# Performance work log

Measured on AMD Instinct MI355X. Metric: run time of the kernel, lower is better.

## Reference

```python
import jax, jax.numpy as jnp
import numpy as np

B, N, D, D_OUT = 8, 2048, 256, 256
LN_EPS = 1e-5
LRELU_SLOPE = 0.01


def setup_inputs() -> dict:
    key = jax.random.key(0)
    ks = jax.random.split(key, 11)
    s_in = 1.0 / np.sqrt(D)
    s_out = 1.0 / np.sqrt(D)
    return {
        "x_local": jax.random.normal(ks[0], (B, N, D), dtype=jnp.float32),
        "Wq": jax.random.uniform(ks[1], (D, D), jnp.float32, -s_in, s_in),
        "bq": jax.random.uniform(ks[2], (D,), jnp.float32, -s_in, s_in),
        "Wk": jax.random.uniform(ks[3], (D, D), jnp.float32, -s_in, s_in),
        "bk": jax.random.uniform(ks[4], (D,), jnp.float32, -s_in, s_in),
        "Wv": jax.random.uniform(ks[5], (D, D), jnp.float32, -s_in, s_in),
        "bv": jax.random.uniform(ks[6], (D,), jnp.float32, -s_in, s_in),
        "Wo": jax.random.uniform(ks[7], (D_OUT, D), jnp.float32, -s_out, s_out),
        "bo": jax.random.uniform(ks[8], (D_OUT,), jnp.float32, -s_out, s_out),
        "ln_gamma": jnp.ones((D_OUT,), jnp.float32),
        "ln_beta": jnp.zeros((D_OUT,), jnp.float32),
    }


def reference(x_local, Wq, bq, Wk, bk, Wv, bv, Wo, bo, ln_gamma, ln_beta):
    # Linear layers (torch convention: y = x @ W.T + b)
    Q = jnp.einsum("bnd,ed->bne", x_local, Wq) + bq
    K = jnp.einsum("bnd,ed->bne", x_local, Wk) + bk
    V = jnp.einsum("bnd,ed->bne", x_local, Wv) + bv
    # Unscaled attention (source applies no 1/sqrt(d))
    scores = jnp.einsum("bnd,bmd->bnm", Q, K)          # [B, N, N]
    attn = jax.nn.softmax(scores, axis=-1)
    loc = jnp.einsum("bnm,bmd->bnd", attn, V)           # [B, N, D]
    # fc_out: Linear -> LayerNorm -> LeakyReLU
    h = jnp.einsum("bnd,ed->bne", loc, Wo) + bo          # [B, N, D_OUT]
    mu = jnp.mean(h, axis=-1, keepdims=True)
    var = jnp.mean(jnp.square(h - mu), axis=-1, keepdims=True)
    hn = (h - mu) / jnp.sqrt(var + LN_EPS) * ln_gamma + ln_beta
    return jnp.where(hn >= 0, hn, LRELU_SLOPE * hn)
```

## Files before the change

kernel.cpp:

```cpp
#include <hip/hip_runtime.h>

typedef unsigned short u16;
typedef __attribute__((ext_vector_type(8))) _Float16 f16x8;
typedef __attribute__((ext_vector_type(4))) float f32x4;

#define MFMA_F16 __builtin_amdgcn_mfma_f32_16x16x32_f16

static __device__ __forceinline__ u16 f2h(float f) {
    return __builtin_bit_cast(u16, (_Float16)f);
}
static __device__ __forceinline__ ushort4 f4_to_h4(const float4 v) {
    ushort4 r;
    r.x = f2h(v.x); r.y = f2h(v.y); r.z = f2h(v.z); r.w = f2h(v.w);
    return r;
}
static __device__ __forceinline__ void gl16(const u16* g, u16* l) {
    __builtin_amdgcn_global_load_lds(
        (__attribute__((address_space(1))) void*)(g),
        (__attribute__((address_space(3))) void*)(l),
        16, 0, 0);
}

__global__ __launch_bounds__(256) void prep_w(
    const float* __restrict__ wq, const float* __restrict__ wk,
    const float* __restrict__ wv, const float* __restrict__ wo,
    const float* __restrict__ x,
    u16* __restrict__ w4, u16* __restrict__ xh)
{
    const int tid = blockIdx.x * 256 + threadIdx.x;
    {
        const float* src = (tid < 16384) ? wq : (tid < 32768) ? wk
                         : (tid < 49152) ? wv : wo;
        ((ushort4*)w4)[tid] = f4_to_h4(((const float4*)src)[tid & 16383]);
    }
#pragma unroll
    for (int i = 0; i < 16; ++i) {
        const int j = i * 65536 + tid;
        ((ushort4*)xh)[j] = f4_to_h4(((const float4*)x)[j]);
    }
}

__global__ __launch_bounds__(256, 3) void proj_qkv(
    const u16* __restrict__ Xh, const u16* __restrict__ w4,
    const float* __restrict__ bq, const float* __restrict__ bk,
    const float* __restrict__ bv,
    u16* __restrict__ Qh, u16* __restrict__ Kh, u16* __restrict__ Vt)
{
    const int z = blockIdx.y;
    const u16* __restrict__ W     = w4 + z * 65536;
    const float* __restrict__ bias = (z == 0) ? bq : (z == 1) ? bk : bv;

    const int m0   = blockIdx.x * 64;
    const int t    = threadIdx.x;
    const int w    = t >> 6;
    const int lane = t & 63;
    const int quad = lane >> 4;
    const int l16  = lane & 15;

    __shared__ __align__(16) u16 smem[20480];

    const int xrow = t >> 2, xpp = t & 3;
    const unsigned xsrc = (unsigned)((m0 + xrow) * 256
                        + ((xpp ^ ((xrow >> 1) & 3)) * 8));
    unsigned wsrc[4];
#pragma unroll
    for (int i = 0; i < 4; ++i) {
        const int j = i * 256 + t;
        const int row = j >> 2, p = j & 3;
        wsrc[i] = (unsigned)(row * 256 + ((p ^ ((row >> 1) & 3)) * 8));
    }

#define PSTAGE(bufsel, kc_) do {                                             \
        u16* B_ = smem + (bufsel) * 10240;                                   \
        gl16(Xh + xsrc + (unsigned)(kc_) * 32, B_ + w * 512);                \
        _Pragma("unroll")                                                    \
        for (int i_ = 0; i_ < 4; ++i_)                                       \
            gl16(W + wsrc[i_] + (unsigned)(kc_) * 32,                        \
                 B_ + 2048 + i_ * 2048 + w * 512);                           \
    } while (0)

    f32x4 acc[16];
#pragma unroll
    for (int i = 0; i < 16; ++i) acc[i] = f32x4{0.f, 0.f, 0.f, 0.f};

    const int rp = (quad ^ ((l16 >> 1) & 3)) * 8;

    PSTAGE(0, 0);

    for (int kc = 0; kc < 8; ++kc) {
        asm volatile("s_waitcnt vmcnt(0)" ::: "memory");
        __builtin_amdgcn_s_barrier();
        __builtin_amdgcn_sched_barrier(0);
        if (kc + 1 < 8) PSTAGE((kc + 1) & 1, kc + 1);
        __builtin_amdgcn_sched_barrier(0);

        const u16* Xb = smem + (kc & 1) * 10240;
        const u16* Wb = Xb + 2048;

        const f16x8 af = *(const f16x8*)&Xb[(w * 16 + l16) * 32 + rp];
        __builtin_amdgcn_s_setprio(1);
#pragma unroll
        for (int nt = 0; nt < 16; ++nt) {
            const f16x8 bf = *(const f16x8*)&Wb[(nt * 16 + l16) * 32 + rp];
            acc[nt] = MFMA_F16(af, bf, acc[nt], 0, 0, 0);
        }
        __builtin_amdgcn_s_setprio(0);
    }
#undef PSTAGE

    __syncthreads();

    if (z < 2) {
        u16* __restrict__ Y = (z == 0) ? Qh : Kh;
#pragma unroll
        for (int nt = 0; nt < 16; ++nt) {
            const int col = nt * 16 + l16;
            const float bb = bias[col];
#pragma unroll
            for (int r = 0; r < 4; ++r)
                smem[(w * 16 + quad * 4 + r) * 264 + col] = f2h(acc[nt][r] + bb);
        }
        __syncthreads();
#pragma unroll
        for (int i = 0; i < 8; ++i) {
            const int ch = i * 256 + t;
            const int row = ch >> 5, cg = ch & 31;
            *(int4*)&Y[(size_t)(m0 + row) * 256 + cg * 8] =
                *(const int4*)&smem[row * 264 + cg * 8];
        }
    } else {
        const int b  = m0 >> 11;
        const int n0 = m0 & 2047;
#pragma unroll
        for (int nt = 0; nt < 16; ++nt) {
            const int col = nt * 16 + l16;
            const float bb = bias[col];
            ushort4 h4;
            h4.x = f2h(acc[nt][0] + bb);
            h4.y = f2h(acc[nt][1] + bb);
            h4.z = f2h(acc[nt][2] + bb);
            h4.w = f2h(acc[nt][3] + bb);
            *(ushort4*)&smem[col * 72 + w * 16 + quad * 4] = h4;
        }
        __syncthreads();
#pragma unroll
        for (int i = 0; i < 8; ++i) {
            const int ch = i * 256 + t;
            const int row = ch >> 3, cg = ch & 7;
            *(int4*)&Vt[(size_t)b * 524288 + (size_t)row * 2048 + n0 + cg * 8] =
                *(const int4*)&smem[row * 72 + cg * 8];
        }
    }
}

__global__ __launch_bounds__(512, 4) void attn(
    const u16* __restrict__ Qh, const u16* __restrict__ Kg,
    const u16* __restrict__ Vt, u16* __restrict__ Op,
    u16* __restrict__ OutS, float* __restrict__ lmpL, float* __restrict__ lmpM)
{
    const int nz = gridDim.z;
    const int z  = blockIdx.z;
    const int ntiles = 64 / nz;
    const int tile0  = ntiles * z;

    const int b  = blockIdx.y;
    const int q0 = blockIdx.x * 128;
    const int t    = threadIdx.x;
    const int w    = t >> 6;
    const int lane = t & 63;
    const int quad = lane >> 4;
    const int l16  = lane & 15;

    __shared__ __align__(16) u16 smem[34816];
    u16* Os = smem;

    f16x8 qf[8];
    {
        const size_t qrow = (size_t)(b * 2048 + q0 + w * 16 + l16) * 256;
#pragma unroll
        for (int kc = 0; kc < 8; ++kc)
            qf[kc] = *(const f16x8*)&Qh[qrow + kc * 32 + quad * 8];
    }

    unsigned kgb[2], vgb[2];
#pragma unroll
    for (int i = 0; i < 2; ++i) {
        const int j  = w * 2 + i;
        const int r  = 2 * j + (lane >> 5);
        const int pr = ((r >> 2) & 3) * 8 + (r >> 4) * 4 + (r & 3);
        const int c  = lane & 31;
        kgb[i] = (unsigned)((b * 2048 + pr) * 256 + ((c ^ (r & 7)) * 8));
        const int rp2 = 8 * j + (lane >> 3);
        const int c8 = lane & 7;
        const int d  = 2 * rp2 + (c8 >> 2);
        const int a  = (c8 & 3) ^ (rp2 & 3);
        vgb[i] = (unsigned)(b * 524288 + d * 2048 + a * 8);
    }

#define STAGE(bufsel, kt_) do {                                              \
        u16* Kb_ = smem + (bufsel) * 16384;                                  \
        u16* Vb_ = Kb_ + 8192;                                               \
        _Pragma("unroll")                                                    \
        for (int i_ = 0; i_ < 2; ++i_) {                                     \
            gl16(Kg + kgb[i_] + (unsigned)(kt_) * 256,                       \
                 Kb_ + (w * 2 + i_) * 512);                                  \
            gl16(Vt + vgb[i_] + (unsigned)(kt_),                             \
                 Vb_ + (w * 2 + i_) * 512);                                  \
        }                                                                    \
    } while (0)

    f32x4 O[16];
#pragma unroll
    for (int i = 0; i < 16; ++i) O[i] = f32x4{0.f, 0.f, 0.f, 0.f};
    float mrow = -1e30f, lrow = 0.f;

    const int vbase = (l16 >> 1) * 64 + (l16 & 1) * 32
                    + ((quad ^ ((l16 >> 1) & 3)) * 8);

    STAGE(0, tile0 * 32);

    for (int it = 0; it < ntiles; ++it) {
        asm volatile("s_waitcnt vmcnt(0)" ::: "memory");
        __builtin_amdgcn_s_barrier();
        __builtin_amdgcn_sched_barrier(0);
        if (it + 1 < ntiles) STAGE((it + 1) & 1, (tile0 + it + 1) * 32);
        __builtin_amdgcn_sched_barrier(0);

        const u16* Kc = smem + (it & 1) * 16384;
        const u16* Vc = Kc + 8192;

        f32x4 S[2];
        S[0] = f32x4{0.f, 0.f, 0.f, 0.f};
        S[1] = f32x4{0.f, 0.f, 0.f, 0.f};
        __builtin_amdgcn_s_setprio(1);
#pragma unroll
        for (int kc = 0; kc < 8; ++kc) {
#pragma unroll
            for (int kn = 0; kn < 2; ++kn) {
                const int r2 = kn * 16 + l16;
                const f16x8 kf = *(const f16x8*)
                    &Kc[r2 * 256 + (((kc * 4 + quad) ^ (l16 & 7)) * 8)];
                S[kn] = MFMA_F16(kf, qf[kc], S[kn], 0, 0, 0);
            }
        }
        __builtin_amdgcn_s_setprio(0);

        float mt = fmaxf(fmaxf(fmaxf(S[0][0], S[0][1]), fmaxf(S[0][2], S[0][3])),
                         fmaxf(fmaxf(S[1][0], S[1][1]), fmaxf(S[1][2], S[1][3])));
        mt = fmaxf(mt, __shfl_xor(mt, 16));
        mt = fmaxf(mt, __shfl_xor(mt, 32));
        if (__any(mt - mrow > 8.f)) {
            const float mnew = fmaxf(mrow, mt);
            const float a = __expf(mrow - mnew);
            lrow *= a;
#pragma unroll
            for (int dv = 0; dv < 16; ++dv)
#pragma unroll
                for (int r = 0; r < 4; ++r) O[dv][r] *= a;
            mrow = mnew;
        }
        f16x8 pfv;
        float s = 0.f;
#pragma unroll
        for (int kn = 0; kn < 2; ++kn)
#pragma unroll
            for (int r = 0; r < 4; ++r) {
                const float e = __expf(S[kn][r] - mrow);
                s += e;
                pfv[kn * 4 + r] = (_Float16)e;
            }
        s += __shfl_xor(s, 16);
        s += __shfl_xor(s, 32);
        lrow += s;

        __builtin_amdgcn_s_setprio(1);
#pragma unroll
        for (int dvt = 0; dvt < 16; ++dvt) {
            const f16x8 vf = *(const f16x8*)&Vc[dvt * 512 + vbase];
            O[dvt] = MFMA_F16(vf, pfv, O[dvt], 0, 0, 0);
        }
        __builtin_amdgcn_s_setprio(0);
    }
#undef STAGE

    __syncthreads();
    {
        const float rl = 1.0f / lrow;
#pragma unroll
        for (int dvt = 0; dvt < 16; ++dvt) {
            ushort4 h4;
            h4.x = f2h(O[dvt][0] * rl);
            h4.y = f2h(O[dvt][1] * rl);
            h4.z = f2h(O[dvt][2] * rl);
            h4.w = f2h(O[dvt][3] * rl);
            *(ushort4*)&Os[(w * 16 + l16) * 264 + dvt * 16 + quad * 4] = h4;
        }
        if (quad == 0) {
            const int grow = b * 2048 + q0 + w * 16 + l16;
            lmpL[z * 16384 + grow] = lrow;
            lmpM[z * 16384 + grow] = mrow;
        }
    }
    __syncthreads();

    {
        const int row = t >> 2;
        if (z < 2) {
            u16* __restrict__ Oz = Op + (size_t)z * 4194304;
#pragma unroll
            for (int i = 0; i < 8; ++i) {
                const int chunk = (t & 3) * 8 + i;
                *(int4*)&Oz[(size_t)(b * 2048 + q0 + row) * 256 + chunk * 8] =
                    *(const int4*)&Os[row * 264 + chunk * 8];
            }
        } else {
            u16* __restrict__ Oz = OutS + (size_t)(z - 2) * 256;
#pragma unroll
            for (int i = 0; i < 8; ++i) {
                const int chunk = (t & 3) * 8 + i;
                *(int4*)&Oz[(size_t)(b * 2048 + q0 + row) * 512 + chunk * 8] =
                    *(const int4*)&Os[row * 264 + chunk * 8];
            }
        }
    }
}

__global__ __launch_bounds__(256, 2) void outproj_ln(
    const u16* __restrict__ Op, const u16* __restrict__ OutS,
    const float* __restrict__ lmpL, const float* __restrict__ lmpM,
    const u16* __restrict__ Woh, const float* __restrict__ bo,
    const float* __restrict__ gamma, const float* __restrict__ beta,
    float* __restrict__ out)
{
    const int m0   = blockIdx.x * 32;
    const int t    = threadIdx.x;
    const int w    = t >> 6;
    const int rw   = w & 1;
    const int cw   = w >> 1;
    const int lane = t & 63;
    const int quad = lane >> 4;
    const int l16  = lane & 15;

    __shared__ __align__(16) u16 Ls[32 * 40];
    __shared__ __align__(16) u16 Ws[256 * 40];
    __shared__ _Float16 wls[4][32];
    __shared__ float part[2][16][2][2];

    if (t < 32) {
        const float l0 = lmpL[m0 + t];
        const float l1 = lmpL[16384 + m0 + t];
        const float l2 = lmpL[32768 + m0 + t];
        const float l3 = lmpL[49152 + m0 + t];
        const float m0v = lmpM[m0 + t];
        const float m1v = lmpM[16384 + m0 + t];
        const float m2v = lmpM[32768 + m0 + t];
        const float m3v = lmpM[49152 + m0 + t];
        const float mm = fmaxf(fmaxf(m0v, m1v), fmaxf(m2v, m3v));
        const float u0 = l0 * __expf(m0v - mm);
        const float u1 = l1 * __expf(m1v - mm);
        const float u2 = l2 * __expf(m2v - mm);
        const float u3 = l3 * __expf(m3v - mm);
        const float inv = 1.0f / (u0 + u1 + u2 + u3);
        wls[0][t] = (_Float16)(u0 * inv);
        wls[1][t] = (_Float16)(u1 * inv);
        wls[2][t] = (_Float16)(u2 * inv);
        wls[3][t] = (_Float16)(u3 * inv);
    }
    __syncthreads();

    f32x4 acc[8];
#pragma unroll
    for (int i = 0; i < 8; ++i) acc[i] = f32x4{0.f, 0.f, 0.f, 0.f};

    for (int kc = 0; kc < 8; ++kc) {
        if (t < 128) {
            const int row = t >> 2, cg = t & 3;
            const size_t off  = (size_t)(m0 + row) * 256 + kc * 32 + cg * 8;
            const size_t offS = (size_t)(m0 + row) * 512 + kc * 32 + cg * 8;
            const f16x8 o0 = __builtin_bit_cast(f16x8, *(const int4*)&Op[off]);
            const f16x8 o1 = __builtin_bit_cast(f16x8, *(const int4*)&Op[4194304 + off]);
            const f16x8 o2 = __builtin_bit_cast(f16x8, *(const int4*)&OutS[offS]);
            const f16x8 o3 = __builtin_bit_cast(f16x8, *(const int4*)&OutS[offS + 256]);
            const _Float16 w0 = wls[0][row], w1 = wls[1][row];
            const _Float16 w2 = wls[2][row], w3 = wls[3][row];
            f16x8 lw;
#pragma unroll
            for (int j = 0; j < 8; ++j)
                lw[j] = o0[j] * w0 + o1[j] * w1 + o2[j] * w2 + o3[j] * w3;
            *(int4*)&Ls[row * 40 + cg * 8] = __builtin_bit_cast(int4, lw);
        }
#pragma unroll
        for (int i = 0; i < 4; ++i) {
            const int ch = i * 256 + t;
            const int row = ch >> 2, cg = ch & 3;
            *(int4*)&Ws[row * 40 + cg * 8] =
                *(const int4*)&Woh[(size_t)row * 256 + kc * 32 + cg * 8];
        }
        __syncthreads();

        const f16x8 af = *(const f16x8*)&Ls[(rw * 16 + l16) * 40 + quad * 8];
#pragma unroll
        for (int nt = 0; nt < 8; ++nt) {
            const f16x8 bf = *(const f16x8*)&Ws[((cw * 8 + nt) * 16 + l16) * 40 + quad * 8];
            acc[nt] = MFMA_F16(af, bf, acc[nt], 0, 0, 0);
        }
        __syncthreads();
    }

    float g[8], bt[8], bb[8];
#pragma unroll
    for (int nt = 0; nt < 8; ++nt) {
        const int col = cw * 128 + nt * 16 + l16;
        bb[nt] = bo[col]; g[nt] = gamma[col]; bt[nt] = beta[col];
    }

    float shv[4], sh2v[4];
#pragma unroll
    for (int r = 0; r < 4; ++r) {
        float sh = 0.f, sh2 = 0.f;
#pragma unroll
        for (int nt = 0; nt < 8; ++nt) {
            const float h = acc[nt][r] + bb[nt];
            sh  += h;
            sh2 += h * h;
        }
        sh  += __shfl_xor(sh, 1);  sh  += __shfl_xor(sh, 2);
        sh  += __shfl_xor(sh, 4);  sh  += __shfl_xor(sh, 8);
        sh2 += __shfl_xor(sh2, 1); sh2 += __shfl_xor(sh2, 2);
        sh2 += __shfl_xor(sh2, 4); sh2 += __shfl_xor(sh2, 8);
        shv[r] = sh; sh2v[r] = sh2;
    }
    if (l16 == 0) {
#pragma unroll
        for (int r = 0; r < 4; ++r) {
            part[rw][quad * 4 + r][cw][0] = shv[r];
            part[rw][quad * 4 + r][cw][1] = sh2v[r];
        }
    }
    __syncthreads();

#pragma unroll
    for (int r = 0; r < 4; ++r) {
        const float sh  = shv[r]  + part[rw][quad * 4 + r][cw ^ 1][0];
        const float sh2 = sh2v[r] + part[rw][quad * 4 + r][cw ^ 1][1];
        const float mu  = sh * (1.f / 256.f);
        const float var = fmaxf(sh2 * (1.f / 256.f) - mu * mu, 0.f);
        const float rs  = rsqrtf(var + 1e-5f);
        const size_t row = (size_t)(m0 + rw * 16 + quad * 4 + r) * 256;
#pragma unroll
        for (int nt = 0; nt < 8; ++nt) {
            const float hn = (acc[nt][r] + bb[nt] - mu) * rs * g[nt] + bt[nt];
            out[row + cw * 128 + nt * 16 + l16] = (hn >= 0.f) ? hn : 0.01f * hn;
        }
    }
}

extern "C" void kernel_launch(void* const* d_in, const int* in_sizes, int n_in,
                              void* d_out, int out_size, void* d_ws, size_t ws_size,
                              hipStream_t stream)
{
    const float* x  = (const float*)d_in[0];
    const float* Wq = (const float*)d_in[1];
    const float* bq = (const float*)d_in[2];
    const float* Wk = (const float*)d_in[3];
    const float* bk = (const float*)d_in[4];
    const float* Wv = (const float*)d_in[5];
    const float* bv = (const float*)d_in[6];
    const float* Wo = (const float*)d_in[7];
    const float* bo = (const float*)d_in[8];
    const float* gm = (const float*)d_in[9];
    const float* bt = (const float*)d_in[10];
    float* out = (float*)d_out;

    u16* W4 = (u16*)d_ws;
    u16* Qh = W4 + 262144;
    u16* Kh = Qh + 4194304;
    u16* Vt = Kh + 4194304;
    u16* Op = Vt + 4194304;
    float* lmpM = (float*)(Op + 2 * 4194304);
    float* lmpL = (float*)W4;
    u16* Woh = W4 + 196608;
    u16* Xh  = (u16*)d_out;
    u16* OutS = (u16*)d_out;

    prep_w     <<<256,            256, 0, stream>>>(Wq, Wk, Wv, Wo, x, W4, Xh);
    proj_qkv   <<<dim3(256, 3),   256, 0, stream>>>(Xh, W4, bq, bk, bv, Qh, Kh, Vt);
    attn       <<<dim3(16, 8, 4), 512, 0, stream>>>(Qh, Kh, Vt, Op, OutS, lmpL, lmpM);
    outproj_ln <<<512,            256, 0, stream>>>(Op, OutS, lmpL, lmpM, Woh, bo, gm, bt, out);
}
```

Before: 185.2 us.

## Retile attention to 64-row blocks, 3-way KV split, and separate K/V staging

Attention blocks shrink to 256 threads covering 64 query rows. The KV split becomes 3-way with uneven tile counts, and a linear block-index swizzle is added. K and V loads are staged separately: K is double-buffered and V single-buffered, with extra barriers so the next V load overlaps the QK of the following tile. The output-projection merge now combines three partials instead of four. The aim is better occupancy and less LDS per block, in exchange for more barriers per tile and less V prefetch depth.

```diff
diff --git a/kernel.cpp b/kernel.cpp
--- a/kernel.cpp
+++ b/kernel.cpp
@@ -153,25 +153,29 @@
     }
 }
 
-__global__ __launch_bounds__(512, 4) void attn(
+__global__ __launch_bounds__(256, 3) void attn(
     const u16* __restrict__ Qh, const u16* __restrict__ Kg,
     const u16* __restrict__ Vt, u16* __restrict__ Op,
     u16* __restrict__ OutS, float* __restrict__ lmpL, float* __restrict__ lmpM)
 {
     const int nz = gridDim.z;
-    const int z  = blockIdx.z;
-    const int ntiles = 64 / nz;
-    const int tile0  = ntiles * z;
-
-    const int b  = blockIdx.y;
-    const int q0 = blockIdx.x * 128;
+    int lin = blockIdx.x + 32 * (blockIdx.y + 8 * blockIdx.z);
+    lin = (lin & 7) * 96 + (lin >> 3);
+    const int q0 = (lin & 31) * 64;
+    const int b  = (lin >> 5) & 7;
+    const int z  = lin >> 8;
+
+    const int tbase = 64 / nz, trem = 64 % nz;
+    const int ntiles = tbase + (z < trem ? 1 : 0);
+    const int tile0  = tbase * z + (z < trem ? z : trem);
+
     const int t    = threadIdx.x;
     const int w    = t >> 6;
     const int lane = t & 63;
     const int quad = lane >> 4;
     const int l16  = lane & 15;
 
-    __shared__ __align__(16) u16 smem[34816];
+    __shared__ __align__(16) u16 smem[24576];
     u16* Os = smem;
 
     f16x8 qf[8];
@@ -182,10 +186,10 @@
             qf[kc] = *(const f16x8*)&Qh[qrow + kc * 32 + quad * 8];
     }
 
-    unsigned kgb[2], vgb[2];
-#pragma unroll
-    for (int i = 0; i < 2; ++i) {
-        const int j  = w * 2 + i;
+    unsigned kgb[4], vgb[4];
+#pragma unroll
+    for (int i = 0; i < 4; ++i) {
+        const int j  = w * 4 + i;
         const int r  = 2 * j + (lane >> 5);
         const int pr = ((r >> 2) & 3) * 8 + (r >> 4) * 4 + (r & 3);
         const int c  = lane & 31;
@@ -197,16 +201,19 @@
         vgb[i] = (unsigned)(b * 524288 + d * 2048 + a * 8);
     }
 
-#define STAGE(bufsel, kt_) do {                                              \
-        u16* Kb_ = smem + (bufsel) * 16384;                                  \
-        u16* Vb_ = Kb_ + 8192;                                               \
+#define STAGE_K(bufsel, kt_) do {                                            \
+        u16* Kb_ = smem + (bufsel) * 8192;                                   \
         _Pragma("unroll")                                                    \
-        for (int i_ = 0; i_ < 2; ++i_) {                                     \
+        for (int i_ = 0; i_ < 4; ++i_)                                       \
             gl16(Kg + kgb[i_] + (unsigned)(kt_) * 256,                       \
-                 Kb_ + (w * 2 + i_) * 512);                                  \
+                 Kb_ + (w * 4 + i_) * 512);                                  \
+    } while (0)
+#define STAGE_V(kt_) do {                                                    \
+        u16* Vb_ = smem + 16384;                                             \
+        _Pragma("unroll")                                                    \
+        for (int i_ = 0; i_ < 4; ++i_)                                       \
             gl16(Vt + vgb[i_] + (unsigned)(kt_),                             \
-                 Vb_ + (w * 2 + i_) * 512);                                  \
-        }                                                                    \
+                 Vb_ + (w * 4 + i_) * 512);                                  \
     } while (0)
 
     f32x4 O[16];
@@ -217,17 +224,17 @@
     const int vbase = (l16 >> 1) * 64 + (l16 & 1) * 32
                     + ((quad ^ ((l16 >> 1) & 3)) * 8);
 
-    STAGE(0, tile0 * 32);
+    STAGE_K(0, tile0 * 32);
+    asm volatile("s_waitcnt vmcnt(0)" ::: "memory");
+    __builtin_amdgcn_s_barrier();
+    __builtin_amdgcn_sched_barrier(0);
+    STAGE_V(tile0 * 32);
+    if (ntiles > 1) STAGE_K(1, (tile0 + 1) * 32);
+    __builtin_amdgcn_sched_barrier(0);
 
     for (int it = 0; it < ntiles; ++it) {
-        asm volatile("s_waitcnt vmcnt(0)" ::: "memory");
-        __builtin_amdgcn_s_barrier();
-        __builtin_amdgcn_sched_barrier(0);
-        if (it + 1 < ntiles) STAGE((it + 1) & 1, (tile0 + it + 1) * 32);
-        __builtin_amdgcn_sched_barrier(0);
-
-        const u16* Kc = smem + (it & 1) * 16384;
-        const u16* Vc = Kc + 8192;
+        const u16* Kc = smem + (it & 1) * 8192;
+        const u16* Vc = smem + 16384;
 
         f32x4 S[2];
         S[0] = f32x4{0.f, 0.f, 0.f, 0.f};
@@ -273,6 +280,14 @@
         s += __shfl_xor(s, 32);
         lrow += s;
 
+        if (it + 1 < ntiles) {
+            asm volatile("s_waitcnt vmcnt(4)" ::: "memory");
+        } else {
+            asm volatile("s_waitcnt vmcnt(0)" ::: "memory");
+        }
+        __builtin_amdgcn_s_barrier();
+        __builtin_amdgcn_sched_barrier(0);
+
         __builtin_amdgcn_s_setprio(1);
 #pragma unroll
         for (int dvt = 0; dvt < 16; ++dvt) {
@@ -280,8 +295,18 @@
             O[dvt] = MFMA_F16(vf, pfv, O[dvt], 0, 0, 0);
         }
         __builtin_amdgcn_s_setprio(0);
-    }
-#undef STAGE
+
+        asm volatile("s_waitcnt vmcnt(0)" ::: "memory");
+        __builtin_amdgcn_s_barrier();
+        __builtin_amdgcn_sched_barrier(0);
+        if (it + 1 < ntiles) {
+            STAGE_V((tile0 + it + 1) * 32);
+            if (it + 2 < ntiles) STAGE_K(it & 1, (tile0 + it + 2) * 32);
+        }
+        __builtin_amdgcn_sched_barrier(0);
+    }
+#undef STAGE_K
+#undef STAGE_V
 
     __syncthreads();
     {
@@ -314,7 +339,7 @@
                     *(const int4*)&Os[row * 264 + chunk * 8];
             }
         } else {
-            u16* __restrict__ Oz = OutS + (size_t)(z - 2) * 256;
+            u16* __restrict__ Oz = OutS;
 #pragma unroll
             for (int i = 0; i < 8; ++i) {
                 const int chunk = (t & 3) * 8 + i;
@@ -343,28 +368,24 @@
 
     __shared__ __align__(16) u16 Ls[32 * 40];
     __shared__ __align__(16) u16 Ws[256 * 40];
-    __shared__ _Float16 wls[4][32];
+    __shared__ _Float16 wls[3][32];
     __shared__ float part[2][16][2][2];
 
     if (t < 32) {
         const float l0 = lmpL[m0 + t];
         const float l1 = lmpL[16384 + m0 + t];
         const float l2 = lmpL[32768 + m0 + t];
-        const float l3 = lmpL[49152 + m0 + t];
         const float m0v = lmpM[m0 + t];
         const float m1v = lmpM[16384 + m0 + t];
         const float m2v = lmpM[32768 + m0 + t];
-        const float m3v = lmpM[49152 + m0 + t];
-        const float mm = fmaxf(fmaxf(m0v, m1v), fmaxf(m2v, m3v));
+        const float mm = fmaxf(fmaxf(m0v, m1v), m2v);
         const float u0 = l0 * __expf(m0v - mm);
         const float u1 = l1 * __expf(m1v - mm);
         const float u2 = l2 * __expf(m2v - mm);
-        const float u3 = l3 * __expf(m3v - mm);
-        const float inv = 1.0f / (u0 + u1 + u2 + u3);
+        const float inv = 1.0f / (u0 + u1 + u2);
         wls[0][t] = (_Float16)(u0 * inv);
         wls[1][t] = (_Float16)(u1 * inv);
         wls[2][t] = (_Float16)(u2 * inv);
-        wls[3][t] = (_Float16)(u3 * inv);
     }
     __syncthreads();
 
@@ -380,13 +401,11 @@
             const f16x8 o0 = __builtin_bit_cast(f16x8, *(const int4*)&Op[off]);
             const f16x8 o1 = __builtin_bit_cast(f16x8, *(const int4*)&Op[4194304 + off]);
             const f16x8 o2 = __builtin_bit_cast(f16x8, *(const int4*)&OutS[offS]);
-            const f16x8 o3 = __builtin_bit_cast(f16x8, *(const int4*)&OutS[offS + 256]);
-            const _Float16 w0 = wls[0][row], w1 = wls[1][row];
-            const _Float16 w2 = wls[2][row], w3 = wls[3][row];
+            const _Float16 w0 = wls[0][row], w1 = wls[1][row], w2 = wls[2][row];
             f16x8 lw;
 #pragma unroll
             for (int j = 0; j < 8; ++j)
-                lw[j] = o0[j] * w0 + o1[j] * w1 + o2[j] * w2 + o3[j] * w3;
+                lw[j] = o0[j] * w0 + o1[j] * w1 + o2[j] * w2;
             *(int4*)&Ls[row * 40 + cg * 8] = __builtin_bit_cast(int4, lw);
         }
 #pragma unroll
@@ -485,6 +504,6 @@
 
     prep_w     <<<256,            256, 0, stream>>>(Wq, Wk, Wv, Wo, x, W4, Xh);
     proj_qkv   <<<dim3(256, 3),   256, 0, stream>>>(Xh, W4, bq, bk, bv, Qh, Kh, Vt);
-    attn       <<<dim3(16, 8, 4), 512, 0, stream>>>(Qh, Kh, Vt, Op, OutS, lmpL, lmpM);
+    attn       <<<dim3(32, 8, 3), 256, 0, stream>>>(Qh, Kh, Vt, Op, OutS, lmpL, lmpM);
     outproj_ln <<<512,            256, 0, stream>>>(Op, OutS, lmpL, lmpM, Woh, bo, gm, bt, out);
 }
```

New measurement: 169.2 us. 1.09x faster.
